# Kernel tuning notes

Hardware: AMD Instinct MI355X
Metric: run time of the kernel (lower is better)

Reference implementation:

```python
import jax, jax.numpy as jnp
import numpy as np

B, N, D, DC, R = 32, 36, 2048, 4, 512  # batch, regions, feat dim, coord dim, fusion rank


def setup_inputs() -> dict:
    key = jax.random.key(0)
    ks = jax.random.split(key, 8)
    s = lambda fan_in: 1.0 / np.sqrt(fan_in)
    return {
        "mm": jax.random.normal(ks[0], (B, N, D), dtype=jnp.float32),
        "coords": jax.random.uniform(ks[1], (B, N, DC), dtype=jnp.float32),
        "U_feat": jax.random.normal(ks[2], (D, R), dtype=jnp.float32) * s(D),
        "V_feat": jax.random.normal(ks[3], (D, R), dtype=jnp.float32) * s(D),
        "P_feat": jax.random.normal(ks[4], (R, D), dtype=jnp.float32) * s(R),
        "U_coord": jax.random.normal(ks[5], (DC, R), dtype=jnp.float32) * s(DC),
        "V_coord": jax.random.normal(ks[6], (DC, R), dtype=jnp.float32) * s(DC),
        "P_coord": jax.random.normal(ks[7], (R, D), dtype=jnp.float32) * s(R),
    }


def reference(mm, coords, U_feat, V_feat, P_feat, U_coord, V_coord, P_coord):
    # Pairwise module: build all (i, j) region pairs, fuse, max-aggregate over j.
    # Original torch code detach_()'s the gathered pair tensors -> stop_gradient here.
    mm_sg = jax.lax.stop_gradient(mm)
    coords_sg = jax.lax.stop_gradient(coords)

    # Coord fusion (MLB-style low-rank multiplicative fusion)
    uc = jnp.einsum("bnc,cr->bnr", coords_sg, U_coord)   # [B,N,R]
    vc = jnp.einsum("bnc,cr->bnr", coords_sg, V_coord)   # [B,N,R]
    zc = jax.nn.relu(uc[:, :, None, :] * vc[:, None, :, :])  # [B,N,N,R]
    Rij = jnp.einsum("bijr,rd->bijd", zc, P_coord)       # [B,N,N,D]

    # Feature fusion
    uf = jnp.einsum("bnd,dr->bnr", mm_sg, U_feat)
    vf = jnp.einsum("bnd,dr->bnr", mm_sg, V_feat)
    zf = jax.nn.relu(uf[:, :, None, :] * vf[:, None, :, :])  # [B,N,N,R]
    Rij = Rij + jnp.einsum("bijr,rd->bijd", zf, P_feat)  # [B,N,N,D]

    # agg['type'] == 'max': reduce over the second region axis (j)
    mm_new = jnp.max(Rij, axis=2)                        # [B,N,D]

    # residual
    return mm_new + mm
```

## Files before the change

### kernel.cpp

```cpp
#include <hip/hip_runtime.h>

#define BI    1152
#define NREG  36
#define DD    2048
#define RR    512
#define KK    1024
#define ZROWS (BI*NREG)
#define MBLK  144
#define NBLK  256
#define ABUF  (MBLK*32)
#define BBUF  (NBLK*32)
#define BUFE  (ABUF+BBUF)

typedef __bf16 bf16;
typedef __bf16 bf16x8 __attribute__((ext_vector_type(8)));
typedef __bf16 bf16x4 __attribute__((ext_vector_type(4)));
typedef float  f32x4  __attribute__((ext_vector_type(4)));

__device__ __forceinline__ void gl_lds16(const void* g, void* l) {
  __builtin_amdgcn_global_load_lds(
      (const __attribute__((address_space(1))) unsigned int*)g,
      (__attribute__((address_space(3))) unsigned int*)l, 16, 0, 0);
}

__global__ void k_prep(const float* __restrict__ mm, const float* __restrict__ coords,
                       const float* __restrict__ U_feat, const float* __restrict__ V_feat,
                       const float* __restrict__ P_feat, const float* __restrict__ U_coord,
                       const float* __restrict__ V_coord, const float* __restrict__ P_coord,
                       bf16* __restrict__ mmb, bf16* __restrict__ UT, bf16* __restrict__ VT,
                       bf16* __restrict__ PTt, float* __restrict__ uc, float* __restrict__ vc) {
  __shared__ float tile[32][33];
  int bid = blockIdx.x, tid = threadIdx.x;
  if (bid < 2304) {
    int i = bid * 256 + tid;
    float4 v = ((const float4*)mm)[i];
    bf16x4 o = {(bf16)v.x, (bf16)v.y, (bf16)v.z, (bf16)v.w};
    ((bf16x4*)mmb)[i] = o;
  } else if (bid < 4352) {
    int rel = bid - 2304;
    int zz = rel >> 10, rr = rel & 1023;
    int c0 = (rr & 15) * 32, r0 = (rr >> 4) * 32;
    const float* in = zz ? V_feat : U_feat;
    bf16* outp = zz ? VT : UT;
    int tx = tid & 31, ty = tid >> 5;
#pragma unroll
    for (int k = 0; k < 4; k++)
      tile[ty + 8 * k][tx] = in[(long)(r0 + ty + 8 * k) * 512 + c0 + tx];
    __syncthreads();
#pragma unroll
    for (int k = 0; k < 4; k++)
      outp[(long)(c0 + ty + 8 * k) * 2048 + r0 + tx] = (bf16)tile[tx][ty + 8 * k];
  } else if (bid < 6400) {
    int rel = bid - 4352;
    int zz = rel >> 10, rr = rel & 1023;
    int c0 = (rr & 63) * 32, r0 = (rr >> 6) * 32;
    const float* in = zz ? P_feat : P_coord;
    int koff = zz * 512;
    int tx = tid & 31, ty = tid >> 5;
#pragma unroll
    for (int k = 0; k < 4; k++)
      tile[ty + 8 * k][tx] = in[(long)(r0 + ty + 8 * k) * 2048 + c0 + tx];
    __syncthreads();
    int kc = (koff + r0) >> 5;
#pragma unroll
    for (int k = 0; k < 4; k++) {
      int d = c0 + ty + 8 * k;
      PTt[((long)kc * 2048 + d) * 32 + tx] = (bf16)tile[tx][ty + 8 * k];
    }
  } else {
    int g = bid - 6400;
    float c0 = coords[g * 4 + 0], c1 = coords[g * 4 + 1];
    float c2 = coords[g * 4 + 2], c3 = coords[g * 4 + 3];
#pragma unroll
    for (int i = 0; i < 2; i++) {
      int r = tid + i * 256;
      uc[g * RR + r] = c0 * U_coord[r] + c1 * U_coord[RR + r] + c2 * U_coord[2 * RR + r] + c3 * U_coord[3 * RR + r];
      vc[g * RR + r] = c0 * V_coord[r] + c1 * V_coord[RR + r] + c2 * V_coord[2 * RR + r] + c3 * V_coord[3 * RR + r];
    }
  }
}

__launch_bounds__(256)
__global__ void k_gemm_uv(const bf16* __restrict__ mmb, const bf16* __restrict__ UT,
                          const bf16* __restrict__ VT, float* __restrict__ uf,
                          float* __restrict__ vf) {
  __shared__ bf16 lds2[2][6144];
  const bf16* Bmat = blockIdx.z ? VT : UT;
  float* outp = blockIdx.z ? vf : uf;
  int m0 = blockIdx.x * 64, n0 = blockIdx.y * 128;
  int tid = threadIdx.x, wave = tid >> 6, lane = tid & 63;
  int l15 = lane & 15, qv = lane >> 4;
  int qp_c = qv ^ ((l15 >> 1) & 3);
  int qs = (lane & 3) ^ ((lane >> 3) & 3);

  const bf16* gA = mmb + (long)(m0 + wave * 16 + (lane >> 2)) * 2048 + qs * 8;
  const bf16* gB = Bmat + (long)(n0 + wave * 32 + (lane >> 2)) * 2048 + qs * 8;
  int lA = wave * 512;
  int lB = 2048 + wave * 1024;

  auto stage = [&](int buf, int k0) {
    bf16* db = &lds2[buf][0];
    gl_lds16(gA + k0, db + lA);
    gl_lds16(gB + k0, db + lB);
    gl_lds16(gB + 16 * 2048 + k0, db + lB + 512);
  };

  f32x4 acc[4][2] = {};
  stage(0, 0);
  for (int k0 = 0; k0 < 2048; k0 += 32) {
    int cur = (k0 >> 5) & 1;
    __syncthreads();
    if (k0 + 32 < 2048) stage(cur ^ 1, k0 + 32);
    bf16x8 a[4], b[2];
#pragma unroll
    for (int mt = 0; mt < 4; mt++)
      a[mt] = *(const bf16x8*)(&lds2[cur][0] + (mt * 16 + l15) * 32 + qp_c * 8);
#pragma unroll
    for (int nt = 0; nt < 2; nt++)
      b[nt] = *(const bf16x8*)(&lds2[cur][2048] + (wave * 32 + nt * 16 + l15) * 32 + qp_c * 8);
#pragma unroll
    for (int mt = 0; mt < 4; mt++)
#pragma unroll
      for (int nt = 0; nt < 2; nt++)
        acc[mt][nt] = __builtin_amdgcn_mfma_f32_16x16x32_bf16(a[mt], b[nt], acc[mt][nt], 0, 0, 0);
  }
#pragma unroll
  for (int mt = 0; mt < 4; mt++)
#pragma unroll
    for (int nt = 0; nt < 2; nt++)
#pragma unroll
      for (int r = 0; r < 4; r++) {
        int row = m0 + mt * 16 + qv * 4 + r;
        int col = n0 + wave * 32 + nt * 16 + l15;
        outp[(long)row * RR + col] = acc[mt][nt][r];
      }
}

__global__ void k_build_z(const float* __restrict__ uc, const float* __restrict__ vc,
                          const float* __restrict__ uf, const float* __restrict__ vf,
                          bf16* __restrict__ z) {
  __shared__ float uL[36 * 128];
  __shared__ float vL[36 * 128];
  int kq = blockIdx.x, b = blockIdx.y, tid = threadIdx.x;
  const float* usrc = (kq < 4) ? uc : uf;
  const float* vsrc = (kq < 4) ? vc : vf;
  int kb = (kq & 3) * 128;
  for (int i = tid; i < 1152; i += 256) {
    int row = i >> 5, kk = (i & 31) * 4;
    long src = (long)(b * 36 + row) * RR + kb + kk;
    *(float4*)&uL[row * 128 + kk] = *(const float4*)(usrc + src);
    *(float4*)&vL[row * 128 + kk] = *(const float4*)(vsrc + src);
  }
  __syncthreads();
  for (int c = tid; c < 41472; c += 256) {
    int kcl = c / 10368;
    int rem = c - kcl * 10368;
    int row = rem >> 3;
    int x4 = rem & 7;
    int gl = row / 36;
    int j = row - gl * 36;
    int kl = kcl * 32 + x4 * 4;
    float4 u4 = *(const float4*)&uL[gl * 128 + kl];
    float4 v4 = *(const float4*)&vL[j * 128 + kl];
    float x0 = fmaxf(u4.x * v4.x, 0.f), x1 = fmaxf(u4.y * v4.y, 0.f);
    float x2 = fmaxf(u4.z * v4.z, 0.f), x3 = fmaxf(u4.w * v4.w, 0.f);
    bf16x4 o = {(bf16)x0, (bf16)x1, (bf16)x2, (bf16)x3};
    int bi = b * 36 + gl;
    long rowp = (long)(bi >> 2) * 144 + j * 4 + (bi & 3);
    *(bf16x4*)(z + ((long)(kq * 4 + kcl) * ZROWS + rowp) * 32 + x4 * 4) = o;
  }
}

__launch_bounds__(256, 2)
__global__ void k_main(const bf16* __restrict__ z, const bf16* __restrict__ PTt,
                       const float* __restrict__ mm, float* __restrict__ out) {
  __shared__ bf16 lds[2 * BUFE];
  int bid = blockIdx.x;
  int x = bid & 7, t = bid >> 3;
  int dt = t & 7, go = (t >> 3) * 8 + x;
  int d0 = dt * NBLK;
  int tid = threadIdx.x, wave = tid >> 6, lane = tid & 63;
  int l15 = lane & 15, qv = lane >> 4;
  int qp_c = qv ^ ((l15 >> 1) & 3);

  int qs = (lane & 3) ^ ((lane >> 3) & 3);
  int lroff = (lane >> 2) * 32 + qs * 8;

  const bf16* gA = z + (long)go * ABUF + wave * 1024 + lroff;
  const bf16* gB = PTt + (long)d0 * 32 + wave * 2048 + lroff;
  int lA = wave * 1024;
  int lB = ABUF + wave * 2048;

  int sbuf = 0;
  auto stage = [&]() {
    bf16* db = lds + sbuf * BUFE;
    gl_lds16(gA, db + lA);
    gl_lds16(gA + 512, db + lA + 512);
    if (wave == 0) gl_lds16(gA + 4096, db + 4096);
    gl_lds16(gB, db + lB);
    gl_lds16(gB + 512, db + lB + 512);
    gl_lds16(gB + 1024, db + lB + 1024);
    gl_lds16(gB + 1536, db + lB + 1536);
    gA += (long)ZROWS * 32;
    gB += 2048L * 32;
    sbuf ^= 1;
  };

  f32x4 acc[9][4] = {};
  stage();
  for (int kc = 0; kc < 32; kc++) {
    __syncthreads();
    if (kc < 31) stage();
    const bf16* cur = lds + (kc & 1) * BUFE;
    bf16x8 b[4];
#pragma unroll
    for (int nt = 0; nt < 4; nt++)
      b[nt] = *(const bf16x8*)(cur + ABUF + (wave * 64 + nt * 16 + l15) * 32 + qp_c * 8);
#pragma unroll
    for (int mt = 0; mt < 9; mt++) {
      bf16x8 av = *(const bf16x8*)(cur + (mt * 16 + l15) * 32 + qp_c * 8);
#pragma unroll
      for (int nt = 0; nt < 4; nt++)
        acc[mt][nt] = __builtin_amdgcn_mfma_f32_16x16x32_bf16(av, b[nt], acc[mt][nt], 0, 0, 0);
    }
  }

#pragma unroll
  for (int nt = 0; nt < 4; nt++) {
    float mx[4];
#pragma unroll
    for (int r = 0; r < 4; r++) {
      mx[r] = acc[0][nt][r];
#pragma unroll
      for (int mt = 1; mt < 9; mt++) mx[r] = fmaxf(mx[r], acc[mt][nt][r]);
      mx[r] = fmaxf(mx[r], __shfl_xor(mx[r], 16, 64));
      mx[r] = fmaxf(mx[r], __shfl_xor(mx[r], 32, 64));
    }
    if (lane < 16) {
      int col = d0 + wave * 64 + nt * 16 + lane;
#pragma unroll
      for (int r = 0; r < 4; r++) {
        long oa = (long)(go * 4 + r) * DD + col;
        out[oa] = mx[r] + mm[oa];
      }
    }
  }
}

extern "C" void kernel_launch(void* const* d_in, const int* in_sizes, int n_in,
                              void* d_out, int out_size, void* d_ws, size_t ws_size,
                              hipStream_t stream) {
  const float* mm     = (const float*)d_in[0];
  const float* coords = (const float*)d_in[1];
  const float* U_feat = (const float*)d_in[2];
  const float* V_feat = (const float*)d_in[3];
  const float* P_feat = (const float*)d_in[4];
  const float* U_coord= (const float*)d_in[5];
  const float* V_coord= (const float*)d_in[6];
  const float* P_coord= (const float*)d_in[7];
  float* out = (float*)d_out;

  char* ws = (char*)d_ws;
  bf16* z   = (bf16*)(ws + 0);
  bf16* PTt = (bf16*)(ws + 84934656);
  bf16* mmb = (bf16*)(ws + 89128960);
  bf16* UT  = (bf16*)(ws + 93847552);
  bf16* VT  = (bf16*)(ws + 95944704);
  float* uf = (float*)(ws + 98041856);
  float* vf = (float*)(ws + 100401152);
  float* uc = (float*)(ws + 102760448);
  float* vc = (float*)(ws + 105119744);

  k_prep<<<dim3(7552), dim3(256), 0, stream>>>(mm, coords, U_feat, V_feat, P_feat,
                                               U_coord, V_coord, P_coord,
                                               mmb, UT, VT, PTt, uc, vc);
  k_gemm_uv<<<dim3(18, 4, 2), dim3(256), 0, stream>>>(mmb, UT, VT, uf, vf);
  k_build_z<<<dim3(8, 32), dim3(256), 0, stream>>>(uc, vc, uf, vf, z);
  k_main<<<dim3(2304), dim3(256), 0, stream>>>(z, PTt, mm, out);
}
```

Measured before the change: 259.7 us.

## Fuse pairwise z construction into main GEMM and store u/v factors as bf16

Removes the separate k_build_z kernel, which wrote a ~85MB bf16 pairwise tensor to global memory. The main GEMM now computes relu(u*v) on the fly from bf16 u/v factors, packs it into registers and writes it into the LDS A-tile for the next k-step, overlapping with the current MFMA work. uc/vc/uf/vf are now stored in bf16, which halves their traffic but adds a rounding step before the product. The cost is recomputation per d-tile block (8x redundancy) and extra VALU work and register pressure inside the main loop.

New measurement: 334.6 us. +28.8%, slower.

```diff
diff --git a/kernel.cpp b/kernel.cpp
--- a/kernel.cpp
+++ b/kernel.cpp
@@ -4,8 +4,6 @@
 #define NREG  36
 #define DD    2048
 #define RR    512
-#define KK    1024
-#define ZROWS (BI*NREG)
 #define MBLK  144
 #define NBLK  256
 #define ABUF  (MBLK*32)
@@ -28,7 +26,7 @@
                        const float* __restrict__ P_feat, const float* __restrict__ U_coord,
                        const float* __restrict__ V_coord, const float* __restrict__ P_coord,
                        bf16* __restrict__ mmb, bf16* __restrict__ UT, bf16* __restrict__ VT,
-                       bf16* __restrict__ PTt, float* __restrict__ uc, float* __restrict__ vc) {
+                       bf16* __restrict__ PTt, bf16* __restrict__ uc, bf16* __restrict__ vc) {
   __shared__ float tile[32][33];
   int bid = blockIdx.x, tid = threadIdx.x;
   if (bid < 2304) {
@@ -74,19 +72,19 @@
 #pragma unroll
     for (int i = 0; i < 2; i++) {
       int r = tid + i * 256;
-      uc[g * RR + r] = c0 * U_coord[r] + c1 * U_coord[RR + r] + c2 * U_coord[2 * RR + r] + c3 * U_coord[3 * RR + r];
-      vc[g * RR + r] = c0 * V_coord[r] + c1 * V_coord[RR + r] + c2 * V_coord[2 * RR + r] + c3 * V_coord[3 * RR + r];
+      uc[g * RR + r] = (bf16)(c0 * U_coord[r] + c1 * U_coord[RR + r] + c2 * U_coord[2 * RR + r] + c3 * U_coord[3 * RR + r]);
+      vc[g * RR + r] = (bf16)(c0 * V_coord[r] + c1 * V_coord[RR + r] + c2 * V_coord[2 * RR + r] + c3 * V_coord[3 * RR + r]);
     }
   }
 }
 
 __launch_bounds__(256)
 __global__ void k_gemm_uv(const bf16* __restrict__ mmb, const bf16* __restrict__ UT,
-                          const bf16* __restrict__ VT, float* __restrict__ uf,
-                          float* __restrict__ vf) {
+                          const bf16* __restrict__ VT, bf16* __restrict__ uf,
+                          bf16* __restrict__ vf) {
   __shared__ bf16 lds2[2][6144];
   const bf16* Bmat = blockIdx.z ? VT : UT;
-  float* outp = blockIdx.z ? vf : uf;
+  bf16* outp = blockIdx.z ? vf : uf;
   int m0 = blockIdx.x * 64, n0 = blockIdx.y * 128;
   int tid = threadIdx.x, wave = tid >> 6, lane = tid & 63;
   int l15 = lane & 15, qv = lane >> 4;
@@ -132,97 +130,97 @@
       for (int r = 0; r < 4; r++) {
         int row = m0 + mt * 16 + qv * 4 + r;
         int col = n0 + wave * 32 + nt * 16 + l15;
-        outp[(long)row * RR + col] = acc[mt][nt][r];
+        outp[(long)row * RR + col] = (bf16)acc[mt][nt][r];
       }
 }
 
-__global__ void k_build_z(const float* __restrict__ uc, const float* __restrict__ vc,
-                          const float* __restrict__ uf, const float* __restrict__ vf,
-                          bf16* __restrict__ z) {
-  __shared__ float uL[36 * 128];
-  __shared__ float vL[36 * 128];
-  int kq = blockIdx.x, b = blockIdx.y, tid = threadIdx.x;
-  const float* usrc = (kq < 4) ? uc : uf;
-  const float* vsrc = (kq < 4) ? vc : vf;
-  int kb = (kq & 3) * 128;
-  for (int i = tid; i < 1152; i += 256) {
-    int row = i >> 5, kk = (i & 31) * 4;
-    long src = (long)(b * 36 + row) * RR + kb + kk;
-    *(float4*)&uL[row * 128 + kk] = *(const float4*)(usrc + src);
-    *(float4*)&vL[row * 128 + kk] = *(const float4*)(vsrc + src);
-  }
-  __syncthreads();
-  for (int c = tid; c < 41472; c += 256) {
-    int kcl = c / 10368;
-    int rem = c - kcl * 10368;
-    int row = rem >> 3;
-    int x4 = rem & 7;
-    int gl = row / 36;
-    int j = row - gl * 36;
-    int kl = kcl * 32 + x4 * 4;
-    float4 u4 = *(const float4*)&uL[gl * 128 + kl];
-    float4 v4 = *(const float4*)&vL[j * 128 + kl];
-    float x0 = fmaxf(u4.x * v4.x, 0.f), x1 = fmaxf(u4.y * v4.y, 0.f);
-    float x2 = fmaxf(u4.z * v4.z, 0.f), x3 = fmaxf(u4.w * v4.w, 0.f);
-    bf16x4 o = {(bf16)x0, (bf16)x1, (bf16)x2, (bf16)x3};
-    int bi = b * 36 + gl;
-    long rowp = (long)(bi >> 2) * 144 + j * 4 + (bi & 3);
-    *(bf16x4*)(z + ((long)(kq * 4 + kcl) * ZROWS + rowp) * 32 + x4 * 4) = o;
-  }
-}
-
 __launch_bounds__(256, 2)
-__global__ void k_main(const bf16* __restrict__ z, const bf16* __restrict__ PTt,
-                       const float* __restrict__ mm, float* __restrict__ out) {
+__global__ void k_main(const bf16* __restrict__ uc, const bf16* __restrict__ vc,
+                       const bf16* __restrict__ uf, const bf16* __restrict__ vf,
+                       const bf16* __restrict__ PTt, const float* __restrict__ mm,
+                       float* __restrict__ out) {
   __shared__ bf16 lds[2 * BUFE];
   int bid = blockIdx.x;
   int x = bid & 7, t = bid >> 3;
   int dt = t & 7, go = (t >> 3) * 8 + x;
   int d0 = dt * NBLK;
+  int b = go / 9;
   int tid = threadIdx.x, wave = tid >> 6, lane = tid & 63;
   int l15 = lane & 15, qv = lane >> 4;
   int qp_c = qv ^ ((l15 >> 1) & 3);
-
   int qs = (lane & 3) ^ ((lane >> 3) & 3);
   int lroff = (lane >> 2) * 32 + qs * 8;
 
-  const bf16* gA = z + (long)go * ABUF + wave * 1024 + lroff;
+  int nseg = (wave == 3) ? 3 : 2;
+  int uofs[3], vofs[3], lofsA[3];
+#pragma unroll
+  for (int i = 0; i < 3; i++) {
+    int s = 2 * wave + i;
+    if (s > 8) s = 8;
+    int row = s * 16 + (lane >> 2);
+    uofs[i] = (go * 4 + (row & 3)) * RR;
+    vofs[i] = (b * 36 + (row >> 2)) * RR;
+    lofsA[i] = s * 512 + lane * 8;
+  }
+  int kq8 = qs * 8;
+
   const bf16* gB = PTt + (long)d0 * 32 + wave * 2048 + lroff;
-  int lA = wave * 1024;
   int lB = ABUF + wave * 2048;
 
-  int sbuf = 0;
-  auto stage = [&]() {
-    bf16* db = lds + sbuf * BUFE;
-    gl_lds16(gA, db + lA);
-    gl_lds16(gA + 512, db + lA + 512);
-    if (wave == 0) gl_lds16(gA + 4096, db + 4096);
-    gl_lds16(gB, db + lB);
-    gl_lds16(gB + 512, db + lB + 512);
-    gl_lds16(gB + 1024, db + lB + 1024);
-    gl_lds16(gB + 1536, db + lB + 1536);
-    gA += (long)ZROWS * 32;
-    gB += 2048L * 32;
-    sbuf ^= 1;
+  auto stageB = [&](int buf, int kt) {
+    bf16* db = lds + buf * BUFE;
+    long kb = (long)kt * (2048L * 32);
+    gl_lds16(gB + kb, db + lB);
+    gl_lds16(gB + kb + 512, db + lB + 512);
+    gl_lds16(gB + kb + 1024, db + lB + 1024);
+    gl_lds16(gB + kb + 1536, db + lB + 1536);
+  };
+  auto loadpack = [&](int kt, bf16x8* o) {
+    const bf16* ub; const bf16* vb; int kk;
+    if (kt < 16) { ub = uc; vb = vc; kk = kt * 32 + kq8; }
+    else         { ub = uf; vb = vf; kk = (kt - 16) * 32 + kq8; }
+#pragma unroll
+    for (int i = 0; i < 3; i++) {
+      if (i < nseg) {
+        bf16x8 u8 = *(const bf16x8*)(ub + uofs[i] + kk);
+        bf16x8 v8 = *(const bf16x8*)(vb + vofs[i] + kk);
+#pragma unroll
+        for (int e = 0; e < 8; e++)
+          o[i][e] = (bf16)fmaxf((float)u8[e] * (float)v8[e], 0.f);
+      }
+    }
+  };
+  auto writez = [&](int buf, const bf16x8* o) {
+    bf16* db = lds + buf * BUFE;
+#pragma unroll
+    for (int i = 0; i < 3; i++)
+      if (i < nseg) *(bf16x8*)(db + lofsA[i]) = o[i];
   };
 
   f32x4 acc[9][4] = {};
-  stage();
+  bf16x8 oz[3];
+  loadpack(0, oz);
+  writez(0, oz);
+  stageB(0, 0);
   for (int kc = 0; kc < 32; kc++) {
     __syncthreads();
-    if (kc < 31) stage();
+    if (kc < 31) {
+      stageB((kc + 1) & 1, kc + 1);
+      loadpack(kc + 1, oz);
+    }
     const bf16* cur = lds + (kc & 1) * BUFE;
-    bf16x8 b[4];
+    bf16x8 bfr[4];
 #pragma unroll
     for (int nt = 0; nt < 4; nt++)
-      b[nt] = *(const bf16x8*)(cur + ABUF + (wave * 64 + nt * 16 + l15) * 32 + qp_c * 8);
+      bfr[nt] = *(const bf16x8*)(cur + ABUF + (wave * 64 + nt * 16 + l15) * 32 + qp_c * 8);
 #pragma unroll
     for (int mt = 0; mt < 9; mt++) {
       bf16x8 av = *(const bf16x8*)(cur + (mt * 16 + l15) * 32 + qp_c * 8);
 #pragma unroll
       for (int nt = 0; nt < 4; nt++)
-        acc[mt][nt] = __builtin_amdgcn_mfma_f32_16x16x32_bf16(av, b[nt], acc[mt][nt], 0, 0, 0);
-    }
+        acc[mt][nt] = __builtin_amdgcn_mfma_f32_16x16x32_bf16(av, bfr[nt], acc[mt][nt], 0, 0, 0);
+    }
+    if (kc < 31) writez((kc + 1) & 1, oz);
   }
 
 #pragma unroll
@@ -261,20 +259,18 @@
   float* out = (float*)d_out;
 
   char* ws = (char*)d_ws;
-  bf16* z   = (bf16*)(ws + 0);
-  bf16* PTt = (bf16*)(ws + 84934656);
-  bf16* mmb = (bf16*)(ws + 89128960);
-  bf16* UT  = (bf16*)(ws + 93847552);
-  bf16* VT  = (bf16*)(ws + 95944704);
-  float* uf = (float*)(ws + 98041856);
-  float* vf = (float*)(ws + 100401152);
-  float* uc = (float*)(ws + 102760448);
-  float* vc = (float*)(ws + 105119744);
+  bf16* PTt = (bf16*)(ws + 0);
+  bf16* mmb = (bf16*)(ws + 4194304);
+  bf16* UT  = (bf16*)(ws + 8912896);
+  bf16* VT  = (bf16*)(ws + 11010048);
+  bf16* uf  = (bf16*)(ws + 13107200);
+  bf16* vf  = (bf16*)(ws + 14286848);
+  bf16* uc  = (bf16*)(ws + 15466496);
+  bf16* vc  = (bf16*)(ws + 16646144);
 
   k_prep<<<dim3(7552), dim3(256), 0, stream>>>(mm, coords, U_feat, V_feat, P_feat,
                                                U_coord, V_coord, P_coord,
                                                mmb, UT, VT, PTt, uc, vc);
   k_gemm_uv<<<dim3(18, 4, 2), dim3(256), 0, stream>>>(mmb, UT, VT, uf, vf);
-  k_build_z<<<dim3(8, 32), dim3(256), 0, stream>>>(uc, vc, uf, vf, z);
-  k_main<<<dim3(2304), dim3(256), 0, stream>>>(z, PTt, mm, out);
-}
+  k_main<<<dim3(2304), dim3(256), 0, stream>>>(uc, vc, uf, vf, PTt, mm, out);
+}
```
